# Kernel optimization log

Hardware: AMD Instinct MI355X
Metric: run time of the kernel (lower is better)

Reference implementation:

```python
import jax, jax.numpy as jnp
import numpy as np

B, N, K, D = 4, 32768, 16, 8  # batch, points, neighbors, output channels
EPS = 1e-6  # BatchNorm eps from module


def setup_inputs() -> dict:
    key = jax.random.key(0)
    ks = jax.random.split(key, 6)
    coords = jax.random.normal(ks[0], (B, N, 3), jnp.float32)
    features = jax.random.normal(ks[1], (B, D, N, 1), jnp.float32)
    knn_idx = jax.random.randint(ks[2], (B, N, K), 0, N, dtype=jnp.int64)
    knn_dist = jax.random.uniform(ks[3], (B, N, K), jnp.float32)
    mask = jnp.ones((B, N), jnp.int32)  # all-valid points
    conv_w = jax.random.normal(ks[4], (D, 10), jnp.float32) * 0.1  # 1x1 Conv2d weight (out,in)
    conv_b = jnp.zeros((D,), jnp.float32)
    bn_gamma = jnp.ones((D,), jnp.float32)
    bn_beta = jnp.zeros((D,), jnp.float32)
    return {
        "coords": coords, "features": features, "knn_idx": knn_idx,
        "knn_dist": knn_dist, "mask": mask, "conv_w": conv_w,
        "conv_b": conv_b, "bn_gamma": bn_gamma, "bn_beta": bn_beta,
    }


def reference(coords, features, knn_idx, knn_dist, mask, conv_w, conv_b, bn_gamma, bn_beta):
    # coords: (B,N,3); knn_idx/knn_dist: (B,N,K); features: (B,D,N,1); mask: (B,N)
    idx = jnp.clip(knn_idx, 0, None)
    # gather neighbor coords per batch: (B,N,K,3)
    neighbors = jax.vmap(lambda c, i: c[i])(coords, idx)
    center = jnp.broadcast_to(coords[:, :, None, :], neighbors.shape)  # (B,N,K,3)
    # masked_fill invalid points' distances with +inf (mask==0)
    dist = jnp.where(mask[:, :, None] == 0, jnp.inf, knn_dist)
    # channel-last concat: [center(3), neighbors(3), diff(3), dist(1)] -> (B,N,K,10)
    feat = jnp.concatenate(
        [center, neighbors, center - neighbors, dist[..., None]], axis=-1)
    # 1x1 conv == per-position linear 10 -> D, output layout (B,D,N,K)
    x = jnp.einsum('bnkc,dc->bdnk', feat, conv_w) + conv_b[None, :, None, None]
    # BatchNorm2d in training mode: biased batch stats over (B,N,K) per channel
    mean = x.mean(axis=(0, 2, 3), keepdims=True)
    var = x.var(axis=(0, 2, 3), keepdims=True)
    x = (x - mean) * jax.lax.rsqrt(var + EPS)
    x = x * bn_gamma[None, :, None, None] + bn_beta[None, :, None, None]
    x = jax.nn.relu(x)
    # expand features (B,D,N,1) -> (B,D,N,K) and concat on channel dim
    f = jnp.broadcast_to(features, (x.shape[0], features.shape[1], x.shape[2], x.shape[3]))
    return jnp.concatenate([x, f], axis=1)  # (B, 2D, N, K)
```

## Files before the change

kernel.cpp:

```cpp
#include <hip/hip_runtime.h>
#include <hip/hip_fp16.h>

#define NB 4
#define NP 32768
#define NK 16
#define ND 8
#define EPSV 1e-6f


__global__ __launch_bounds__(256) void lse_pass1(
    const float* __restrict__ coords,
    const float* __restrict__ features,
    const int*   __restrict__ knn_idx,
    const float* __restrict__ knn_dist,
    const int*   __restrict__ mask,
    const float* __restrict__ conv_w,
    const float* __restrict__ conv_b,
    float*       __restrict__ accum,
    __half*      __restrict__ xstage,
    float*       __restrict__ out)
{
    const int gid = blockIdx.x * 256 + threadIdx.x;
    const int b   = gid >> 17;
    const int r   = gid & (NP * 4 - 1);
    const int n   = r >> 2;
    const int k0  = (r & 3) * 4;

    float a0[ND], a1[ND], a2[ND], e0[ND], e1[ND], e2[ND], w9[ND], cb[ND];
#pragma unroll
    for (int d = 0; d < ND; ++d) {
        const float* w = conv_w + d * 10;
        float w0 = w[0], w1 = w[1], w2 = w[2];
        float w3 = w[3], w4 = w[4], w5 = w[5];
        float w6 = w[6], w7 = w[7], w8 = w[8];
        a0[d] = w0 + w6; a1[d] = w1 + w7; a2[d] = w2 + w8;
        e0[d] = w3 - w6; e1[d] = w4 - w7; e2[d] = w5 - w8;
        w9[d] = w[9];    cb[d] = conv_b[d];
    }

    const float* cbase = coords + (size_t)b * NP * 3;
    const float  cx = cbase[n * 3 + 0];
    const float  cy = cbase[n * 3 + 1];
    const float  cz = cbase[n * 3 + 2];

    const size_t p  = ((size_t)(b * NP + n)) * NK + k0;
    const int4   id = *(const int4*)(knn_idx + p);
    float4       dv = *(const float4*)(knn_dist + p);
    if (mask[b * NP + n] == 0) {
        dv.x = dv.y = dv.z = dv.w = __builtin_inff();
    }

    const int   js[4] = {id.x < 0 ? 0 : id.x, id.y < 0 ? 0 : id.y,
                         id.z < 0 ? 0 : id.z, id.w < 0 ? 0 : id.w};
    const float ds[4] = {dv.x, dv.y, dv.z, dv.w};

    float xv[4][ND];
    float sum[ND], sq[ND];
#pragma unroll
    for (int d = 0; d < ND; ++d) { sum[d] = 0.f; sq[d] = 0.f; }

#pragma unroll
    for (int t = 0; t < 4; ++t) {
        const float* nb = cbase + (size_t)js[t] * 3;
        const float  nx = nb[0], ny = nb[1], nz = nb[2];
#pragma unroll
        for (int d = 0; d < ND; ++d) {
            float x = fmaf(a0[d], cx, fmaf(a1[d], cy, fmaf(a2[d], cz,
                      fmaf(e0[d], nx, fmaf(e1[d], ny, fmaf(e2[d], nz,
                      fmaf(w9[d], ds[t], cb[d])))))));
            xv[t][d] = x;
            sum[d] += x;
            sq[d]   = fmaf(x, x, sq[d]);
        }
    }

    if (xstage) {
#pragma unroll
        for (int d = 0; d < ND; ++d) {
            __half2* o2 = (__half2*)(xstage +
                ((((size_t)(b * ND + d)) * NP + n) << 4) + k0);
            o2[0] = __floats2half2_rn(xv[0][d], xv[1][d]);
            o2[1] = __floats2half2_rn(xv[2][d], xv[3][d]);
        }
    } else {
#pragma unroll
        for (int d = 0; d < ND; ++d) {
            *(float4*)(out + ((((size_t)(b * 2 * ND + d)) * NP + n) << 4) + k0) =
                make_float4(xv[0][d], xv[1][d], xv[2][d], xv[3][d]);
        }
    }

    const float* fb = features + (size_t)b * ND * NP;
#pragma unroll
    for (int d = 0; d < ND; ++d) {
        const float v = fb[d * NP + n];
        *(float4*)(out + ((((size_t)(b * 2 * ND + ND + d)) * NP + n) << 4) + k0) =
            make_float4(v, v, v, v);
    }

#pragma unroll
    for (int d = 0; d < ND; ++d) {
        float s = sum[d], s2 = sq[d];
#pragma unroll
        for (int off = 32; off > 0; off >>= 1) {
            s  += __shfl_down(s,  off);
            s2 += __shfl_down(s2, off);
        }
        sum[d] = s; sq[d] = s2;
    }
    __shared__ float lds[4][16];
    const int wave = threadIdx.x >> 6, lane = threadIdx.x & 63;
    if (lane == 0) {
#pragma unroll
        for (int d = 0; d < ND; ++d) {
            lds[wave][d]     = sum[d];
            lds[wave][8 + d] = sq[d];
        }
    }
    __syncthreads();
    if (threadIdx.x < 16) {
        float v = lds[0][threadIdx.x] + lds[1][threadIdx.x]
                + lds[2][threadIdx.x] + lds[3][threadIdx.x];
        atomicAdd(&accum[threadIdx.x], v);
    }
}

__global__ __launch_bounds__(256) void lse_pass2(
    const float*  __restrict__ accum,
    const float*  __restrict__ bn_gamma,
    const float*  __restrict__ bn_beta,
    const __half* __restrict__ xstage,
    float*        __restrict__ out)
{
    const int    gid = blockIdx.x * 256 + threadIdx.x;
    const size_t s0  = (size_t)gid * 8;
    const int    d   = (int)((s0 >> 19) & 7);
    const int    b   = (int)(s0 >> 22);
    const size_t inp = s0 & ((1u << 19) - 1);
    const size_t o   = (((size_t)(b * 2 * ND + d)) << 19) | inp;

    const float invM = 1.0f / (float)(NB * NP * NK);
    const float mean = accum[d] * invM;
    const float var  = fmaf(-mean, mean, accum[8 + d] * invM);
    const float g    = bn_gamma[d] * rsqrtf(var + EPSV);
    const float sh   = fmaf(-mean, g, bn_beta[d]);

    float x[8];
    if (xstage) {
        const float4 raw = *(const float4*)(xstage + s0);
        const __half2* h = (const __half2*)&raw;
#pragma unroll
        for (int q = 0; q < 4; ++q) {
            float2 f = __half22float2(h[q]);
            x[2 * q]     = f.x;
            x[2 * q + 1] = f.y;
        }
    } else {
        const float4 v0 = *(const float4*)(out + o);
        const float4 v1 = *(const float4*)(out + o + 4);
        x[0] = v0.x; x[1] = v0.y; x[2] = v0.z; x[3] = v0.w;
        x[4] = v1.x; x[5] = v1.y; x[6] = v1.z; x[7] = v1.w;
    }

    float4 r0, r1;
    r0.x = fmaxf(fmaf(x[0], g, sh), 0.f);
    r0.y = fmaxf(fmaf(x[1], g, sh), 0.f);
    r0.z = fmaxf(fmaf(x[2], g, sh), 0.f);
    r0.w = fmaxf(fmaf(x[3], g, sh), 0.f);
    r1.x = fmaxf(fmaf(x[4], g, sh), 0.f);
    r1.y = fmaxf(fmaf(x[5], g, sh), 0.f);
    r1.z = fmaxf(fmaf(x[6], g, sh), 0.f);
    r1.w = fmaxf(fmaf(x[7], g, sh), 0.f);
    *(float4*)(out + o)     = r0;
    *(float4*)(out + o + 4) = r1;
}

extern "C" void kernel_launch(void* const* d_in, const int* in_sizes, int n_in,
                              void* d_out, int out_size, void* d_ws, size_t ws_size,
                              hipStream_t stream) {
    const float* coords   = (const float*)d_in[0];
    const float* features = (const float*)d_in[1];
    const int*   knn_idx  = (const int*)  d_in[2];
    const float* knn_dist = (const float*)d_in[3];
    const int*   mask     = (const int*)  d_in[4];
    const float* conv_w   = (const float*)d_in[5];
    const float* conv_b   = (const float*)d_in[6];
    const float* bn_gamma = (const float*)d_in[7];
    const float* bn_beta  = (const float*)d_in[8];
    float* out   = (float*)d_out;
    float* accum = (float*)d_ws;

    hipMemsetAsync(d_ws, 0, 64, stream);

    __half* xstage = nullptr;
    const size_t need = 256 + (size_t)NB * ND * NP * NK * sizeof(__half);
    if (ws_size >= need) xstage = (__half*)((char*)d_ws + 256);

    lse_pass1<<<(NB * NP * 4) / 256, 256, 0, stream>>>(
        coords, features, knn_idx, knn_dist, mask, conv_w, conv_b,
        accum, xstage, out);

    lse_pass2<<<(NB * ND * NP * NK / 8) / 256, 256, 0, stream>>>(
        accum, bn_gamma, bn_beta, xstage, out);
}
```

Baseline: 196.3 us.

## Recompute conv outputs instead of staging them, and pad coords to float4

```diff
diff --git a/kernel.cpp b/kernel.cpp
--- a/kernel.cpp
+++ b/kernel.cpp
@@ -1,5 +1,4 @@
 #include <hip/hip_runtime.h>
-#include <hip/hip_fp16.h>
 
 #define NB 4
 #define NP 32768
@@ -8,17 +7,37 @@
 #define EPSV 1e-6f
 
 
-__global__ __launch_bounds__(256) void lse_pass1(
-    const float* __restrict__ coords,
-    const float* __restrict__ features,
-    const int*   __restrict__ knn_idx,
-    const float* __restrict__ knn_dist,
-    const int*   __restrict__ mask,
-    const float* __restrict__ conv_w,
-    const float* __restrict__ conv_b,
-    float*       __restrict__ accum,
-    __half*      __restrict__ xstage,
-    float*       __restrict__ out)
+__global__ __launch_bounds__(256) void pad_coords(const float* __restrict__ coords,
+                                                  float4* __restrict__ c4) {
+    int i = blockIdx.x * 256 + threadIdx.x;
+    if (i < NB * NP) {
+        const float* s = coords + (size_t)i * 3;
+        c4[i] = make_float4(s[0], s[1], s[2], 0.f);
+    }
+}
+
+#define LOAD_FOLDED_W()                                            \
+    float a0[ND], a1[ND], a2[ND], e0[ND], e1[ND], e2[ND], w9[ND], cb[ND]; \
+    _Pragma("unroll")                                              \
+    for (int d = 0; d < ND; ++d) {                                 \
+        const float* w = conv_w + d * 10;                          \
+        float w0 = w[0], w1 = w[1], w2 = w[2];                     \
+        float w3 = w[3], w4 = w[4], w5 = w[5];                     \
+        float w6 = w[6], w7 = w[7], w8 = w[8];                     \
+        a0[d] = w0 + w6; a1[d] = w1 + w7; a2[d] = w2 + w8;         \
+        e0[d] = w3 - w6; e1[d] = w4 - w7; e2[d] = w5 - w8;         \
+        w9[d] = w[9];    cb[d] = conv_b[d];                        \
+    }
+
+__global__ __launch_bounds__(256) void lse_stats(
+    const float*  __restrict__ coords,
+    const int*    __restrict__ knn_idx,
+    const float*  __restrict__ knn_dist,
+    const int*    __restrict__ mask,
+    const float*  __restrict__ conv_w,
+    const float*  __restrict__ conv_b,
+    const float4* __restrict__ c4,
+    float*        __restrict__ accum)
 {
     const int gid = blockIdx.x * 256 + threadIdx.x;
     const int b   = gid >> 17;
@@ -26,76 +45,44 @@
     const int n   = r >> 2;
     const int k0  = (r & 3) * 4;
 
-    float a0[ND], a1[ND], a2[ND], e0[ND], e1[ND], e2[ND], w9[ND], cb[ND];
-#pragma unroll
-    for (int d = 0; d < ND; ++d) {
-        const float* w = conv_w + d * 10;
-        float w0 = w[0], w1 = w[1], w2 = w[2];
-        float w3 = w[3], w4 = w[4], w5 = w[5];
-        float w6 = w[6], w7 = w[7], w8 = w[8];
-        a0[d] = w0 + w6; a1[d] = w1 + w7; a2[d] = w2 + w8;
-        e0[d] = w3 - w6; e1[d] = w4 - w7; e2[d] = w5 - w8;
-        w9[d] = w[9];    cb[d] = conv_b[d];
-    }
-
-    const float* cbase = coords + (size_t)b * NP * 3;
-    const float  cx = cbase[n * 3 + 0];
-    const float  cy = cbase[n * 3 + 1];
-    const float  cz = cbase[n * 3 + 2];
+    LOAD_FOLDED_W();
+
+    const float*  cbase = coords + (size_t)b * NP * 3;
+    const float4* c4b   = c4 ? c4 + (size_t)b * NP : nullptr;
+
+    float cx, cy, cz;
+    if (c4b) { float4 cc = c4b[n]; cx = cc.x; cy = cc.y; cz = cc.z; }
+    else     { cx = cbase[n*3]; cy = cbase[n*3+1]; cz = cbase[n*3+2]; }
 
     const size_t p  = ((size_t)(b * NP + n)) * NK + k0;
     const int4   id = *(const int4*)(knn_idx + p);
     float4       dv = *(const float4*)(knn_dist + p);
-    if (mask[b * NP + n] == 0) {
-        dv.x = dv.y = dv.z = dv.w = __builtin_inff();
-    }
+    if (mask[b * NP + n] == 0) dv.x = dv.y = dv.z = dv.w = __builtin_inff();
 
     const int   js[4] = {id.x < 0 ? 0 : id.x, id.y < 0 ? 0 : id.y,
                          id.z < 0 ? 0 : id.z, id.w < 0 ? 0 : id.w};
     const float ds[4] = {dv.x, dv.y, dv.z, dv.w};
 
-    float xv[4][ND];
     float sum[ND], sq[ND];
 #pragma unroll
     for (int d = 0; d < ND; ++d) { sum[d] = 0.f; sq[d] = 0.f; }
 
 #pragma unroll
     for (int t = 0; t < 4; ++t) {
-        const float* nb = cbase + (size_t)js[t] * 3;
-        const float  nx = nb[0], ny = nb[1], nz = nb[2];
+        float nx, ny, nz;
+        if (c4b) { float4 nn = c4b[js[t]]; nx = nn.x; ny = nn.y; nz = nn.z; }
+        else {
+            const float* nb = cbase + (size_t)js[t] * 3;
+            nx = nb[0]; ny = nb[1]; nz = nb[2];
+        }
 #pragma unroll
         for (int d = 0; d < ND; ++d) {
             float x = fmaf(a0[d], cx, fmaf(a1[d], cy, fmaf(a2[d], cz,
                       fmaf(e0[d], nx, fmaf(e1[d], ny, fmaf(e2[d], nz,
                       fmaf(w9[d], ds[t], cb[d])))))));
-            xv[t][d] = x;
             sum[d] += x;
             sq[d]   = fmaf(x, x, sq[d]);
         }
-    }
-
-    if (xstage) {
-#pragma unroll
-        for (int d = 0; d < ND; ++d) {
-            __half2* o2 = (__half2*)(xstage +
-                ((((size_t)(b * ND + d)) * NP + n) << 4) + k0);
-            o2[0] = __floats2half2_rn(xv[0][d], xv[1][d]);
-            o2[1] = __floats2half2_rn(xv[2][d], xv[3][d]);
-        }
-    } else {
-#pragma unroll
-        for (int d = 0; d < ND; ++d) {
-            *(float4*)(out + ((((size_t)(b * 2 * ND + d)) * NP + n) << 4) + k0) =
-                make_float4(xv[0][d], xv[1][d], xv[2][d], xv[3][d]);
-        }
-    }
-
-    const float* fb = features + (size_t)b * ND * NP;
-#pragma unroll
-    for (int d = 0; d < ND; ++d) {
-        const float v = fb[d * NP + n];
-        *(float4*)(out + ((((size_t)(b * 2 * ND + ND + d)) * NP + n) << 4) + k0) =
-            make_float4(v, v, v, v);
     }
 
 #pragma unroll
@@ -125,54 +112,90 @@
     }
 }
 
-__global__ __launch_bounds__(256) void lse_pass2(
-    const float*  __restrict__ accum,
+__global__ __launch_bounds__(256) void lse_main(
+    const float*  __restrict__ coords,
+    const float*  __restrict__ features,
+    const int*    __restrict__ knn_idx,
+    const float*  __restrict__ knn_dist,
+    const int*    __restrict__ mask,
+    const float*  __restrict__ conv_w,
+    const float*  __restrict__ conv_b,
     const float*  __restrict__ bn_gamma,
     const float*  __restrict__ bn_beta,
-    const __half* __restrict__ xstage,
+    const float*  __restrict__ accum,
+    const float4* __restrict__ c4,
     float*        __restrict__ out)
 {
-    const int    gid = blockIdx.x * 256 + threadIdx.x;
-    const size_t s0  = (size_t)gid * 8;
-    const int    d   = (int)((s0 >> 19) & 7);
-    const int    b   = (int)(s0 >> 22);
-    const size_t inp = s0 & ((1u << 19) - 1);
-    const size_t o   = (((size_t)(b * 2 * ND + d)) << 19) | inp;
+    const int gid = blockIdx.x * 256 + threadIdx.x;
+    const int b   = gid >> 17;
+    const int r   = gid & (NP * 4 - 1);
+    const int n   = r >> 2;
+    const int k0  = (r & 3) * 4;
 
     const float invM = 1.0f / (float)(NB * NP * NK);
-    const float mean = accum[d] * invM;
-    const float var  = fmaf(-mean, mean, accum[8 + d] * invM);
-    const float g    = bn_gamma[d] * rsqrtf(var + EPSV);
-    const float sh   = fmaf(-mean, g, bn_beta[d]);
-
-    float x[8];
-    if (xstage) {
-        const float4 raw = *(const float4*)(xstage + s0);
-        const __half2* h = (const __half2*)&raw;
-#pragma unroll
-        for (int q = 0; q < 4; ++q) {
-            float2 f = __half22float2(h[q]);
-            x[2 * q]     = f.x;
-            x[2 * q + 1] = f.y;
-        }
-    } else {
-        const float4 v0 = *(const float4*)(out + o);
-        const float4 v1 = *(const float4*)(out + o + 4);
-        x[0] = v0.x; x[1] = v0.y; x[2] = v0.z; x[3] = v0.w;
-        x[4] = v1.x; x[5] = v1.y; x[6] = v1.z; x[7] = v1.w;
-    }
-
-    float4 r0, r1;
-    r0.x = fmaxf(fmaf(x[0], g, sh), 0.f);
-    r0.y = fmaxf(fmaf(x[1], g, sh), 0.f);
-    r0.z = fmaxf(fmaf(x[2], g, sh), 0.f);
-    r0.w = fmaxf(fmaf(x[3], g, sh), 0.f);
-    r1.x = fmaxf(fmaf(x[4], g, sh), 0.f);
-    r1.y = fmaxf(fmaf(x[5], g, sh), 0.f);
-    r1.z = fmaxf(fmaf(x[6], g, sh), 0.f);
-    r1.w = fmaxf(fmaf(x[7], g, sh), 0.f);
-    *(float4*)(out + o)     = r0;
-    *(float4*)(out + o + 4) = r1;
+    float scale[ND], shift[ND];
+#pragma unroll
+    for (int d = 0; d < ND; ++d) {
+        float mean = accum[d] * invM;
+        float var  = fmaf(-mean, mean, accum[8 + d] * invM);
+        float g    = bn_gamma[d] * rsqrtf(var + EPSV);
+        scale[d] = g;
+        shift[d] = fmaf(-mean, g, bn_beta[d]);
+    }
+
+    LOAD_FOLDED_W();
+
+    const float*  cbase = coords + (size_t)b * NP * 3;
+    const float4* c4b   = c4 ? c4 + (size_t)b * NP : nullptr;
+
+    float cx, cy, cz;
+    if (c4b) { float4 cc = c4b[n]; cx = cc.x; cy = cc.y; cz = cc.z; }
+    else     { cx = cbase[n*3]; cy = cbase[n*3+1]; cz = cbase[n*3+2]; }
+
+    const size_t p  = ((size_t)(b * NP + n)) * NK + k0;
+    const int4   id = *(const int4*)(knn_idx + p);
+    float4       dv = *(const float4*)(knn_dist + p);
+    if (mask[b * NP + n] == 0) dv.x = dv.y = dv.z = dv.w = __builtin_inff();
+
+    const int   js[4] = {id.x < 0 ? 0 : id.x, id.y < 0 ? 0 : id.y,
+                         id.z < 0 ? 0 : id.z, id.w < 0 ? 0 : id.w};
+    const float ds[4] = {dv.x, dv.y, dv.z, dv.w};
+
+    float xv[4][ND];
+#pragma unroll
+    for (int t = 0; t < 4; ++t) {
+        float nx, ny, nz;
+        if (c4b) { float4 nn = c4b[js[t]]; nx = nn.x; ny = nn.y; nz = nn.z; }
+        else {
+            const float* nb = cbase + (size_t)js[t] * 3;
+            nx = nb[0]; ny = nb[1]; nz = nb[2];
+        }
+#pragma unroll
+        for (int d = 0; d < ND; ++d) {
+            xv[t][d] = fmaf(a0[d], cx, fmaf(a1[d], cy, fmaf(a2[d], cz,
+                       fmaf(e0[d], nx, fmaf(e1[d], ny, fmaf(e2[d], nz,
+                       fmaf(w9[d], ds[t], cb[d])))))));
+        }
+    }
+
+    const size_t pos = ((size_t)n << 4) + k0;
+#pragma unroll
+    for (int d = 0; d < ND; ++d) {
+        float4 v;
+        v.x = fmaxf(fmaf(xv[0][d], scale[d], shift[d]), 0.f);
+        v.y = fmaxf(fmaf(xv[1][d], scale[d], shift[d]), 0.f);
+        v.z = fmaxf(fmaf(xv[2][d], scale[d], shift[d]), 0.f);
+        v.w = fmaxf(fmaf(xv[3][d], scale[d], shift[d]), 0.f);
+        *(float4*)(out + (((size_t)(b * 2 * ND + d)) << 19) + pos) = v;
+    }
+
+    const float* fb = features + (size_t)b * ND * NP;
+#pragma unroll
+    for (int d = 0; d < ND; ++d) {
+        const float f = fb[d * NP + n];
+        *(float4*)(out + (((size_t)(b * 2 * ND + ND + d)) << 19) + pos) =
+            make_float4(f, f, f, f);
+    }
 }
 
 extern "C" void kernel_launch(void* const* d_in, const int* in_sizes, int n_in,
@@ -192,14 +215,17 @@
 
     hipMemsetAsync(d_ws, 0, 64, stream);
 
-    __half* xstage = nullptr;
-    const size_t need = 256 + (size_t)NB * ND * NP * NK * sizeof(__half);
-    if (ws_size >= need) xstage = (__half*)((char*)d_ws + 256);
-
-    lse_pass1<<<(NB * NP * 4) / 256, 256, 0, stream>>>(
+    const float4* c4 = nullptr;
+    if (ws_size >= 256 + (size_t)NB * NP * sizeof(float4)) {
+        float4* c4w = (float4*)((char*)d_ws + 256);
+        pad_coords<<<(NB * NP + 255) / 256, 256, 0, stream>>>(coords, c4w);
+        c4 = c4w;
+    }
+
+    lse_stats<<<(NB * NP * 4) / 256, 256, 0, stream>>>(
+        coords, knn_idx, knn_dist, mask, conv_w, conv_b, c4, accum);
+
+    lse_main<<<(NB * NP * 4) / 256, 256, 0, stream>>>(
         coords, features, knn_idx, knn_dist, mask, conv_w, conv_b,
-        accum, xstage, out);
-
-    lse_pass2<<<(NB * ND * NP * NK / 8) / 256, 256, 0, stream>>>(
-        accum, bn_gamma, bn_beta, xstage, out);
-}
+        bn_gamma, bn_beta, accum, c4, out);
+}
```

After: 212.4 us. +8.2%, slower.
